# Kernel optimization log

Hardware: AMD Instinct MI355X
Metric: run time of the kernel (lower is better)

## Reference

```python
import jax, jax.numpy as jnp
import numpy as np

N, E, F_IN, H = 100000, 3200000, 256, 32

def gcn_conv(x, src, dst, w, W, b):
    # PyG GCNConv with edge weights and added self-loops (weight 1), symmetric norm
    xw = x @ W                                                # [N, H]
    deg = jax.ops.segment_sum(w, dst, num_segments=N) + 1.0   # includes self-loop
    dis = jax.lax.rsqrt(deg)                                  # deg >= 1, safe
    norm = dis[src] * w * dis[dst]                            # [E]
    agg = jax.ops.segment_sum(norm[:, None] * xw[src], dst, num_segments=N)
    agg = agg + (dis * dis)[:, None] * xw                     # self-loop term
    return agg + b


def setup_inputs() -> dict:
    key = jax.random.key(0)
    ks = jax.random.split(key, 20)
    z = lambda n: jnp.zeros((n,), jnp.float32)
    p = lambda i, shape, s: jax.random.normal(ks[i], shape, jnp.float32) * s
    return {
        "x": jax.random.normal(ks[0], (N, F_IN), jnp.float32),
        "edge_index": jax.random.randint(ks[1], (2, E), 0, N),
        "edge_weight": jax.random.uniform(ks[2], (E,), jnp.float32),
        "prev_hidden_state": jax.random.normal(ks[3], (N, H), jnp.float32),
        # GCNConv weights (stored [in, out]) + post-aggregation biases
        "W_z": p(4, (F_IN, H), 0.05), "b_z": z(H),
        "W_r": p(5, (F_IN, H), 0.05), "b_r": z(H),
        "W_h": p(6, (F_IN, H), 0.05), "b_h": z(H),
        # GRU gate linears Linear(2H, H), stored [2H, H]
        "Lz_W": p(7, (2 * H, H), 0.1), "Lz_b": z(H),
        "Lr_W": p(8, (2 * H, H), 0.1), "Lr_b": z(H),
        "Lh_W": p(9, (2 * H, H), 0.1), "Lh_b": z(H),
        # readout Linear(H, 1)
        "head_W": p(10, (H, 1), 0.1), "head_b": z(1),
    }


def reference(x, edge_index, edge_weight, prev_hidden_state,
              W_z, b_z, W_r, b_r, W_h, b_h,
              Lz_W, Lz_b, Lr_W, Lr_b, Lh_W, Lh_b,
              head_W, head_b):
    src, dst = edge_index[0], edge_index[1]
    Hp = prev_hidden_state
    Z = jax.nn.sigmoid(
        jnp.concatenate([gcn_conv(x, src, dst, edge_weight, W_z, b_z), Hp], 1) @ Lz_W + Lz_b)
    R = jax.nn.sigmoid(
        jnp.concatenate([gcn_conv(x, src, dst, edge_weight, W_r, b_r), Hp], 1) @ Lr_W + Lr_b)
    H_tilde = jnp.tanh(
        jnp.concatenate([gcn_conv(x, src, dst, edge_weight, W_h, b_h), Hp * R], 1) @ Lh_W + Lh_b)
    h = Z * Hp + (1.0 - Z) * H_tilde
    y = jax.nn.relu(h) @ head_W + head_b
    return (y, h)
```

## Files before the change

kernel.cpp:

```cpp
#include <hip/hip_runtime.h>
#include <math.h>

#define N_NODES 100000
#define F_INDIM 256
#define NB 391
#define BCAP 9216

__device__ __forceinline__ unsigned bf16pack(float a, float b) {
  unsigned ua = __float_as_uint(a);
  ua += 0x7FFFu + ((ua >> 16) & 1u);
  unsigned ub = __float_as_uint(b);
  ub += 0x7FFFu + ((ub >> 16) & 1u);
  return (ub & 0xFFFF0000u) | (ua >> 16);
}
__device__ __forceinline__ float lo16(unsigned v) { return __uint_as_float(v << 16); }
__device__ __forceinline__ float hi16(unsigned v) { return __uint_as_float(v & 0xFFFF0000u); }

using bf16x8 = __attribute__((ext_vector_type(8))) short;
using f32x4  = __attribute__((ext_vector_type(4))) float;

__global__ __launch_bounds__(512) void gemm_bin(
    const float* __restrict__ x,
    const float* __restrict__ Wz, const float* __restrict__ Wr, const float* __restrict__ Wh,
    unsigned* __restrict__ XWb,
    const int* __restrict__ ei, const float* __restrict__ w,
    int* __restrict__ bucketCursor, uint2* __restrict__ staged, int E) {
  __shared__ unsigned smem[12672];
  const int t = threadIdx.x;
  const int m = blockIdx.x % 5;
  if (m < 2) {
    int* lc    = (int*)smem;
    int* lbase = (int*)smem + 512;
    if (t < NB) lc[t] = 0;
    __syncthreads();
    const int bid = (blockIdx.x / 5) * 2 + m;
    const int base = bid * 6144;
#pragma unroll
    for (int i = 0; i < 12; i++) {
      int e = base + i * 512 + t;
      if (e < E) atomicAdd(&lc[((unsigned)ei[E + e]) >> 8], 1);
    }
    __syncthreads();
    if (t < NB) {
      int c = lc[t];
      lbase[t] = c ? atomicAdd(&bucketCursor[t], c) : 0;
    }
    __syncthreads();
    if (t < NB) lc[t] = 0;
    __syncthreads();
#pragma unroll
    for (int i = 0; i < 12; i++) {
      int e = base + i * 512 + t;
      if (e < E) {
        unsigned dst = (unsigned)ei[E + e];
        int b = dst >> 8;
        int r = lbase[b] + atomicAdd(&lc[b], 1);
        if (r < BCAP)
          staged[(size_t)b * BCAP + r] =
              make_uint2((unsigned)ei[e] | ((dst & 255u) << 17), __float_as_uint(w[e]));
      }
    }
    return;
  }
  const int gid = (blockIdx.x / 5) * 3 + (m - 2);
  const int row0 = gid * 128;
  if (row0 >= N_NODES) return;
  ushort* sWt = (ushort*)smem;
  {
    const float* Ws[3] = {Wz, Wr, Wh};
#pragma unroll
    for (int mm = 0; mm < 3; mm++) {
      const float* Wp = Ws[mm];
      for (int i = t; i < 8192; i += 512) {
        int k = i >> 5, c = i & 31;
        unsigned uv = __float_as_uint(Wp[i]);
        uv += 0x7FFFu + ((uv >> 16) & 1u);
        sWt[(mm * 32 + c) * 264 + k] = (ushort)(uv >> 16);
      }
    }
  }
  __syncthreads();
  const int wv = t >> 6;
  const int l = t & 63;
  const int nl = l & 15;
  const int kg = l >> 4;
  int arow = row0 + wv * 16 + nl;
  int arowc = arow < N_NODES ? arow : N_NODES - 1;
  f32x4 acc[6];
#pragma unroll
  for (int c = 0; c < 6; c++) acc[c] = (f32x4){0.f, 0.f, 0.f, 0.f};
  const float* xrow = x + (size_t)arowc * F_INDIM + kg * 8;
#pragma unroll
  for (int ks = 0; ks < 8; ks++) {
    float4 xa = *(const float4*)(xrow + ks * 32);
    float4 xb = *(const float4*)(xrow + ks * 32 + 4);
    uint4 au;
    au.x = bf16pack(xa.x, xa.y);
    au.y = bf16pack(xa.z, xa.w);
    au.z = bf16pack(xb.x, xb.y);
    au.w = bf16pack(xb.z, xb.w);
    bf16x8 af = *(bf16x8*)&au;
#pragma unroll
    for (int c = 0; c < 6; c++) {
      const ushort* bp = sWt + (c * 16 + nl) * 264 + ks * 32 + kg * 8;
      bf16x8 bf = *(const bf16x8*)bp;
      acc[c] = __builtin_amdgcn_mfma_f32_16x16x32_bf16(af, bf, acc[c], 0, 0, 0);
    }
  }
#pragma unroll
  for (int c = 0; c < 6; c++) {
#pragma unroll
    for (int r = 0; r < 4; r++) {
      float v = acc[c][r];
      float o = __shfl_xor(v, 1);
      int orow = row0 + wv * 16 + kg * 4 + r;
      if ((nl & 1) == 0 && orow < N_NODES)
        XWb[(size_t)orow * 48 + c * 8 + (nl >> 1)] = bf16pack(v, o);
    }
  }
}

__global__ __launch_bounds__(256) void finalize(
    const uint2* __restrict__ staged, const int* __restrict__ bucketCursor,
    uint2* __restrict__ e2, int* __restrict__ rowstart, int* __restrict__ cntA,
    float* __restrict__ dis) {
  __shared__ int fc[256];
  __shared__ float fd[256];
  __shared__ int fscan[256];
  __shared__ int fcur[256];
  const int t = threadIdx.x;
  const int b = blockIdx.x;
  const size_t lo = (size_t)b * BCAP;
  int M = bucketCursor[b]; if (M > BCAP) M = BCAP;
  fc[t] = 0; fd[t] = 0.f;
  __syncthreads();
  for (int i = t; i < M; i += 256) {
    uint2 ed = staged[lo + i];
    int fl = (ed.x >> 17) & 255;
    atomicAdd(&fc[fl], 1);
    atomicAdd(&fd[fl], __uint_as_float(ed.y));
  }
  __syncthreads();
  int v = fc[t];
  fscan[t] = v;
  __syncthreads();
  for (int off = 1; off < 256; off <<= 1) {
    int xv = (t >= off) ? fscan[t - off] : 0;
    __syncthreads();
    fscan[t] += xv;
    __syncthreads();
  }
  int excl = fscan[t] - v;
  int node = (b << 8) + t;
  if (node < N_NODES) {
    rowstart[node] = (int)lo + excl;
    cntA[node] = v;
    dis[node] = rsqrtf(fd[t] + 1.0f);
  }
  fcur[t] = excl;
  __syncthreads();
  for (int i = t; i < M; i += 256) {
    uint2 ed = staged[lo + i];
    int fl = (ed.x >> 17) & 255;
    int p = atomicAdd(&fcur[fl], 1);
    e2[lo + p] = make_uint2(ed.x & 0x1FFFFu, ed.y);
  }
}

#define FMA8(vv, nn)                                              \
  a0 = fmaf(nn, lo16(vv.x), a0); a1 = fmaf(nn, hi16(vv.x), a1);   \
  a2 = fmaf(nn, lo16(vv.y), a2); a3 = fmaf(nn, hi16(vv.y), a3);   \
  a4 = fmaf(nn, lo16(vv.z), a4); a5 = fmaf(nn, hi16(vv.z), a5);   \
  a6 = fmaf(nn, lo16(vv.w), a6); a7 = fmaf(nn, hi16(vv.w), a7);

__global__ __launch_bounds__(256, 6) void gru_gather(
    const uint2* __restrict__ e2, const int* __restrict__ rowstart,
    const int* __restrict__ cnt, const unsigned* __restrict__ XWb,
    const float* __restrict__ dis, const float* __restrict__ Hp,
    const float* __restrict__ bz, const float* __restrict__ br, const float* __restrict__ bh,
    const float* __restrict__ LzW, const float* __restrict__ Lzb,
    const float* __restrict__ LrW, const float* __restrict__ Lrb,
    const float* __restrict__ LhW, const float* __restrict__ Lhb,
    const float* __restrict__ hW, const float* __restrict__ hb,
    float* __restrict__ outY, float* __restrict__ outH, int N) {
  __shared__ unsigned sLz[1024], sLr[1024], sLh[1024];
  __shared__ float aggTmp[4][5][96];
  __shared__ float sb96[96];
  __shared__ float sLzb[32], sLrb[32], sLhb[32], shW[32];
  __shared__ float2 sg2[4][48];
  __shared__ float shp[4][32], shr[4][32];
  __shared__ float shb;
  const int t = threadIdx.x;
  for (int i = t; i < 1024; i += 256) {
    int jj = i & 31, k2 = i >> 5;
    sLz[i] = bf16pack(LzW[(2 * k2) * 32 + jj], LzW[(2 * k2 + 1) * 32 + jj]);
    sLr[i] = bf16pack(LrW[(2 * k2) * 32 + jj], LrW[(2 * k2 + 1) * 32 + jj]);
    sLh[i] = bf16pack(LhW[(2 * k2) * 32 + jj], LhW[(2 * k2 + 1) * 32 + jj]);
  }
  if (t < 32) {
    sb96[t] = bz[t]; sb96[32 + t] = br[t]; sb96[64 + t] = bh[t];
    sLzb[t] = Lzb[t]; sLrb[t] = Lrb[t]; sLhb[t] = Lhb[t]; shW[t] = hW[t];
  }
  if (t == 0) shb = hb[0];
  __syncthreads();
  const int ws = t >> 6;
  const int l = t & 63;
  const int lp = (l < 48) ? l : 47;
  const int j = l & 31;
  const int half = l >> 5;
  const int sl = (l < 60) ? (l / 12) : 4;
  const int q  = (l < 60) ? (l % 12) : 11;
  const float* sgf = (const float*)&sg2[ws][0];
  int wid = blockIdx.x * 4 + ws;
  int nw = gridDim.x * 4;
  for (int n = wid; n < N; n += nw) {
    const int start = rowstart[n];
    const int c = cnt[n];
    const float d = dis[n];
    float a0 = 0.f, a1 = 0.f, a2 = 0.f, a3 = 0.f;
    float a4 = 0.f, a5 = 0.f, a6 = 0.f, a7 = 0.f;
    for (int e0 = 0; e0 < c; e0 += 60) {
      int srcv = 0; float pw = 0.f;
      if (l < 60 && e0 + l < c) {
        uint2 ed = e2[start + e0 + l];
        srcv = (int)ed.x;
        pw = __uint_as_float(ed.y) * dis[srcv];
      }
      int mm = c - e0; if (mm > 60) mm = 60;
      for (int k0 = 0; k0 < mm; k0 += 10) {
        int iA = k0 + sl, iB = k0 + 5 + sl;
        int sA = __shfl(srcv, iA), sB = __shfl(srcv, iB);
        float nA = __shfl(pw, iA), nB = __shfl(pw, iB);
        uint4 vA = *(const uint4*)(XWb + sA * 48 + (q << 2));
        uint4 vB = *(const uint4*)(XWb + sB * 48 + (q << 2));
        FMA8(vA, nA);
        FMA8(vB, nB);
      }
    }
    if (l < 60) {
      float4* dst4 = (float4*)&aggTmp[ws][sl][q * 8];
      dst4[0] = make_float4(a0, a1, a2, a3);
      dst4[1] = make_float4(a4, a5, a6, a7);
    }
    float g0 = 0.f, g1 = 0.f;
#pragma unroll
    for (int ss = 0; ss < 5; ss++) {
      float2 v2 = *(const float2*)&aggTmp[ws][ss][2 * lp];
      g0 += v2.x; g1 += v2.y;
    }
    g0 *= d; g1 *= d;
    {
      unsigned v = XWb[n * 48 + lp];
      float d2 = d * d;
      g0 = fmaf(d2, lo16(v), g0) + sb96[2 * lp];
      g1 = fmaf(d2, hi16(v), g1) + sb96[2 * lp + 1];
    }
    if (l < 48) sg2[ws][l] = make_float2(g0, g1);
    float hpj = 0.f;
    if (l < 32) { hpj = Hp[(size_t)n * 32 + l]; shp[ws][l] = hpj; }
    const unsigned* Wm = half ? sLr : sLz;
    const float* gsel = half ? (sgf + 32) : sgf;
    float val = half ? sLrb[j] : sLzb[j];
#pragma unroll
    for (int k2 = 0; k2 < 16; k2++) {
      unsigned wv = Wm[k2 * 32 + j];
      val = fmaf(gsel[2 * k2],     lo16(wv), val);
      val = fmaf(gsel[2 * k2 + 1], hi16(wv), val);
    }
#pragma unroll
    for (int k2 = 16; k2 < 32; k2++) {
      unsigned wv = Wm[k2 * 32 + j];
      val = fmaf(shp[ws][2 * k2 - 32], lo16(wv), val);
      val = fmaf(shp[ws][2 * k2 - 31], hi16(wv), val);
    }
    float gate = 1.f / (1.f + __expf(-val));
    if (half) shr[ws][j] = shp[ws][j] * gate;
    float s = half ? 0.f : sLhb[j];
#pragma unroll
    for (int k2 = 0; k2 < 16; k2++) {
      int kk2 = half ? (k2 + 16) : k2;
      unsigned wv = sLh[kk2 * 32 + j];
      float x0 = half ? shr[ws][2 * k2]     : sgf[64 + 2 * k2];
      float x1 = half ? shr[ws][2 * k2 + 1] : sgf[64 + 2 * k2 + 1];
      s = fmaf(x0, lo16(wv), s);
      s = fmaf(x1, hi16(wv), s);
    }
    s += __shfl_xor(s, 32);
    if (!half) {
      float ht = tanhf(s);
      float h = gate * hpj + (1.f - gate) * ht;
      outH[(size_t)n * 32 + j] = h;
      float cacc = fmaxf(h, 0.f) * shW[j];
#pragma unroll
      for (int off = 16; off > 0; off >>= 1) cacc += __shfl_xor(cacc, off, 32);
      if (j == 0) outY[n] = cacc + shb;
    }
  }
}

extern "C" void kernel_launch(void* const* d_in, const int* in_sizes, int n_in,
                              void* d_out, int out_size, void* d_ws, size_t ws_size,
                              hipStream_t stream) {
  const float* x    = (const float*)d_in[0];
  const int*   ei   = (const int*)d_in[1];
  const float* w    = (const float*)d_in[2];
  const float* Hp   = (const float*)d_in[3];
  const float* Wz   = (const float*)d_in[4];
  const float* bz   = (const float*)d_in[5];
  const float* Wr   = (const float*)d_in[6];
  const float* br   = (const float*)d_in[7];
  const float* Wh   = (const float*)d_in[8];
  const float* bh   = (const float*)d_in[9];
  const float* LzW  = (const float*)d_in[10];
  const float* Lzb  = (const float*)d_in[11];
  const float* LrW  = (const float*)d_in[12];
  const float* Lrb  = (const float*)d_in[13];
  const float* LhW  = (const float*)d_in[14];
  const float* Lhb  = (const float*)d_in[15];
  const float* hW   = (const float*)d_in[16];
  const float* hb   = (const float*)d_in[17];

  const int N = N_NODES;
  const int E = in_sizes[2];

  char* p = (char*)d_ws;
  unsigned* XWb   = (unsigned*)p;  p += (size_t)(N * 48 + 64) * 4;
  uint2*    staged= (uint2*)p;     p += (size_t)NB * BCAP * 8;
  uint2*    e2    = (uint2*)p;     p += (size_t)NB * BCAP * 8;
  int* rowstart   = (int*)p;       p += (size_t)N * 4;
  int* cnt        = (int*)p;       p += (size_t)N * 4;
  float* dis      = (float*)p;     p += (size_t)N * 4;
  int* bucketCursor = (int*)p;     p += (NB + 1) * 4;

  float* outY = (float*)d_out;
  float* outH = outY + N;

  hipMemsetAsync(bucketCursor, 0, (NB + 1) * sizeof(int), stream);

  gemm_bin<<<1305, 512, 0, stream>>>(x, Wz, Wr, Wh, XWb, ei, w,
                                     bucketCursor, staged, E);
  finalize<<<NB, 256, 0, stream>>>(staged, bucketCursor, e2, rowstart, cnt, dis);
  gru_gather<<<1536, 256, 0, stream>>>(e2, rowstart, cnt, XWb, dis, Hp,
                                       bz, br, bh,
                                       LzW, Lzb, LrW, Lrb, LhW, Lhb,
                                       hW, hb, outY, outH, N);
}
```

Before: 232.0 us.

## Gather neighbor features from an FP8 copy of XW instead of BF16

The finalize kernel now also converts the BF16 XW matrix into a packed FP8 (e4m3) copy. The edge gather reads 24 bytes per source row instead of 48 and decodes them with hardware fp8-to-f32 conversion. Lanes are remapped so 6 lanes cover a row and 10 edges are processed per step, with a cross-lane shuffle reduction before the shared-memory sum. The aim is to halve the dominant random-gather traffic, at the cost of an extra conversion pass and a notable loss of precision in the aggregated features.

```diff
diff --git a/kernel.cpp b/kernel.cpp
--- a/kernel.cpp
+++ b/kernel.cpp
@@ -18,6 +18,7 @@
 
 using bf16x8 = __attribute__((ext_vector_type(8))) short;
 using f32x4  = __attribute__((ext_vector_type(4))) float;
+using f32x2  = __attribute__((ext_vector_type(2))) float;
 
 __global__ __launch_bounds__(512) void gemm_bin(
     const float* __restrict__ x,
@@ -123,7 +124,8 @@
 __global__ __launch_bounds__(256) void finalize(
     const uint2* __restrict__ staged, const int* __restrict__ bucketCursor,
     uint2* __restrict__ e2, int* __restrict__ rowstart, int* __restrict__ cntA,
-    float* __restrict__ dis) {
+    float* __restrict__ dis,
+    const unsigned* __restrict__ XWb, unsigned* __restrict__ XW8) {
   __shared__ int fc[256];
   __shared__ float fd[256];
   __shared__ int fscan[256];
@@ -165,17 +167,22 @@
     int p = atomicAdd(&fcur[fl], 1);
     e2[lo + p] = make_uint2(ed.x & 0x1FFFFu, ed.y);
   }
-}
-
-#define FMA8(vv, nn)                                              \
-  a0 = fmaf(nn, lo16(vv.x), a0); a1 = fmaf(nn, hi16(vv.x), a1);   \
-  a2 = fmaf(nn, lo16(vv.y), a2); a3 = fmaf(nn, hi16(vv.y), a3);   \
-  a4 = fmaf(nn, lo16(vv.z), a4); a5 = fmaf(nn, hi16(vv.z), a5);   \
-  a6 = fmaf(nn, lo16(vv.w), a6); a7 = fmaf(nn, hi16(vv.w), a7);
+  for (int i = t; i < 256 * 24; i += 256) {
+    int row = (b << 8) + (i / 24);
+    if (row >= N_NODES) break;
+    int od = i % 24;
+    unsigned u0 = XWb[(size_t)row * 48 + od * 2];
+    unsigned u1 = XWb[(size_t)row * 48 + od * 2 + 1];
+    int r = __builtin_amdgcn_cvt_pk_fp8_f32(lo16(u0), hi16(u0), 0, false);
+    r = __builtin_amdgcn_cvt_pk_fp8_f32(lo16(u1), hi16(u1), r, true);
+    XW8[(size_t)row * 24 + od] = (unsigned)r;
+  }
+}
 
 __global__ __launch_bounds__(256, 6) void gru_gather(
     const uint2* __restrict__ e2, const int* __restrict__ rowstart,
     const int* __restrict__ cnt, const unsigned* __restrict__ XWb,
+    const unsigned* __restrict__ XW8,
     const float* __restrict__ dis, const float* __restrict__ Hp,
     const float* __restrict__ bz, const float* __restrict__ br, const float* __restrict__ bh,
     const float* __restrict__ LzW, const float* __restrict__ Lzb,
@@ -208,8 +215,8 @@
   const int lp = (l < 48) ? l : 47;
   const int j = l & 31;
   const int half = l >> 5;
-  const int sl = (l < 60) ? (l / 12) : 4;
-  const int q  = (l < 60) ? (l % 12) : 11;
+  const int s10 = (l < 60) ? (l / 6) : 9;
+  const int q6  = (l < 60) ? (l % 6) : 5;
   const float* sgf = (const float*)&sg2[ws][0];
   int wid = blockIdx.x * 4 + ws;
   int nw = gridDim.x * 4;
@@ -217,30 +224,53 @@
     const int start = rowstart[n];
     const int c = cnt[n];
     const float d = dis[n];
-    float a0 = 0.f, a1 = 0.f, a2 = 0.f, a3 = 0.f;
-    float a4 = 0.f, a5 = 0.f, a6 = 0.f, a7 = 0.f;
+    float a[16];
+#pragma unroll
+    for (int i = 0; i < 16; i++) a[i] = 0.f;
     for (int e0 = 0; e0 < c; e0 += 60) {
-      int srcv = 0; float pw = 0.f;
+      unsigned srcv = 0; float pw = 0.f;
       if (l < 60 && e0 + l < c) {
         uint2 ed = e2[start + e0 + l];
-        srcv = (int)ed.x;
+        srcv = ed.x;
         pw = __uint_as_float(ed.y) * dis[srcv];
       }
       int mm = c - e0; if (mm > 60) mm = 60;
-      for (int k0 = 0; k0 < mm; k0 += 10) {
-        int iA = k0 + sl, iB = k0 + 5 + sl;
-        int sA = __shfl(srcv, iA), sB = __shfl(srcv, iB);
+      for (int k0 = 0; k0 < mm; k0 += 20) {
+        int iA = k0 + s10, iB = k0 + 10 + s10;
+        unsigned sA = __shfl(srcv, iA), sB = __shfl(srcv, iB);
         float nA = __shfl(pw, iA), nB = __shfl(pw, iB);
-        uint4 vA = *(const uint4*)(XWb + sA * 48 + (q << 2));
-        uint4 vB = *(const uint4*)(XWb + sB * 48 + (q << 2));
-        FMA8(vA, nA);
-        FMA8(vB, nB);
+        uint4 vA = *(const uint4*)(XW8 + (size_t)sA * 24 + (q6 << 2));
+        uint4 vB = *(const uint4*)(XW8 + (size_t)sB * 24 + (q6 << 2));
+#pragma unroll
+        for (int dd = 0; dd < 4; dd++) {
+          unsigned wd = (dd == 0) ? vA.x : (dd == 1) ? vA.y : (dd == 2) ? vA.z : vA.w;
+          f32x2 f01 = __builtin_amdgcn_cvt_pk_f32_fp8((int)wd, false);
+          f32x2 f23 = __builtin_amdgcn_cvt_pk_f32_fp8((int)wd, true);
+          a[dd * 4 + 0] = fmaf(nA, f01[0], a[dd * 4 + 0]);
+          a[dd * 4 + 1] = fmaf(nA, f01[1], a[dd * 4 + 1]);
+          a[dd * 4 + 2] = fmaf(nA, f23[0], a[dd * 4 + 2]);
+          a[dd * 4 + 3] = fmaf(nA, f23[1], a[dd * 4 + 3]);
+        }
+#pragma unroll
+        for (int dd = 0; dd < 4; dd++) {
+          unsigned wd = (dd == 0) ? vB.x : (dd == 1) ? vB.y : (dd == 2) ? vB.z : vB.w;
+          f32x2 f01 = __builtin_amdgcn_cvt_pk_f32_fp8((int)wd, false);
+          f32x2 f23 = __builtin_amdgcn_cvt_pk_f32_fp8((int)wd, true);
+          a[dd * 4 + 0] = fmaf(nB, f01[0], a[dd * 4 + 0]);
+          a[dd * 4 + 1] = fmaf(nB, f01[1], a[dd * 4 + 1]);
+          a[dd * 4 + 2] = fmaf(nB, f23[0], a[dd * 4 + 2]);
+          a[dd * 4 + 3] = fmaf(nB, f23[1], a[dd * 4 + 3]);
+        }
       }
     }
-    if (l < 60) {
-      float4* dst4 = (float4*)&aggTmp[ws][sl][q * 8];
-      dst4[0] = make_float4(a0, a1, a2, a3);
-      dst4[1] = make_float4(a4, a5, a6, a7);
+#pragma unroll
+    for (int i = 0; i < 16; i++) a[i] += __shfl(a[i], l + 30);
+    if (l < 30) {
+      float4* dst4 = (float4*)&aggTmp[ws][s10][q6 * 16];
+      dst4[0] = make_float4(a[0], a[1], a[2], a[3]);
+      dst4[1] = make_float4(a[4], a[5], a[6], a[7]);
+      dst4[2] = make_float4(a[8], a[9], a[10], a[11]);
+      dst4[3] = make_float4(a[12], a[13], a[14], a[15]);
     }
     float g0 = 0.f, g1 = 0.f;
 #pragma unroll
@@ -250,7 +280,7 @@
     }
     g0 *= d; g1 *= d;
     {
-      unsigned v = XWb[n * 48 + lp];
+      unsigned v = XWb[(size_t)n * 48 + lp];
       float d2 = d * d;
       g0 = fmaf(d2, lo16(v), g0) + sb96[2 * lp];
       g1 = fmaf(d2, hi16(v), g1) + sb96[2 * lp + 1];
@@ -325,6 +355,7 @@
 
   char* p = (char*)d_ws;
   unsigned* XWb   = (unsigned*)p;  p += (size_t)(N * 48 + 64) * 4;
+  unsigned* XW8   = (unsigned*)p;  p += (size_t)(N * 24 + 64) * 4;
   uint2*    staged= (uint2*)p;     p += (size_t)NB * BCAP * 8;
   uint2*    e2    = (uint2*)p;     p += (size_t)NB * BCAP * 8;
   int* rowstart   = (int*)p;       p += (size_t)N * 4;
@@ -339,8 +370,9 @@
 
   gemm_bin<<<1305, 512, 0, stream>>>(x, Wz, Wr, Wh, XWb, ei, w,
                                      bucketCursor, staged, E);
-  finalize<<<NB, 256, 0, stream>>>(staged, bucketCursor, e2, rowstart, cnt, dis);
-  gru_gather<<<1536, 256, 0, stream>>>(e2, rowstart, cnt, XWb, dis, Hp,
+  finalize<<<NB, 256, 0, stream>>>(staged, bucketCursor, e2, rowstart, cnt, dis,
+                                   XWb, XW8);
+  gru_gather<<<1536, 256, 0, stream>>>(e2, rowstart, cnt, XWb, XW8, dis, Hp,
                                        bz, br, bh,
                                        LzW, Lzb, LrW, Lrb, LhW, Lhb,
                                        hW, hb, outY, outH, N);
```

Measured after the change: 306.8 us. +32.3%, slower.

## Move edge binning to its own kernel and co-schedule finalize with the GEMM

Applied to the files above, without the earlier changes.

Edge binning now runs as a standalone kernel that keeps dst indices in registers instead of reloading them. The bucket finalize pass (count, scan, scatter) is merged into the GEMM kernel, interleaved by block index, so finalize work overlaps the x@W GEMM rather than running as a separate launch afterwards. Finalize blocks now use 512 threads with half idle during the scan. The kernel count stays the same, but binning no longer overlaps the GEMM. The gather also switches to size_t index arithmetic.

```diff
diff --git a/kernel.cpp b/kernel.cpp
--- a/kernel.cpp
+++ b/kernel.cpp
@@ -19,50 +19,101 @@
 using bf16x8 = __attribute__((ext_vector_type(8))) short;
 using f32x4  = __attribute__((ext_vector_type(4))) float;
 
-__global__ __launch_bounds__(512) void gemm_bin(
+__global__ __launch_bounds__(512) void bin_kernel(
+    const int* __restrict__ ei, const float* __restrict__ w,
+    int* __restrict__ bucketCursor, uint2* __restrict__ staged, int E) {
+  __shared__ int lc[512];
+  __shared__ int lbase[512];
+  const int t = threadIdx.x;
+  if (t < NB) lc[t] = 0;
+  __syncthreads();
+  const int base = blockIdx.x * 6144;
+  int dstv[12];
+#pragma unroll
+  for (int i = 0; i < 12; i++) {
+    int e = base + i * 512 + t;
+    dstv[i] = (e < E) ? ei[E + e] : -1;
+    if (dstv[i] >= 0) atomicAdd(&lc[((unsigned)dstv[i]) >> 8], 1);
+  }
+  __syncthreads();
+  if (t < NB) {
+    int c = lc[t];
+    lbase[t] = c ? atomicAdd(&bucketCursor[t], c) : 0;
+  }
+  __syncthreads();
+  if (t < NB) lc[t] = 0;
+  __syncthreads();
+#pragma unroll
+  for (int i = 0; i < 12; i++) {
+    int e = base + i * 512 + t;
+    if (dstv[i] >= 0) {
+      unsigned dst = (unsigned)dstv[i];
+      int b = dst >> 8;
+      int r = lbase[b] + atomicAdd(&lc[b], 1);
+      if (r < BCAP)
+        staged[(size_t)b * BCAP + r] =
+            make_uint2((unsigned)ei[e] | ((dst & 255u) << 17), __float_as_uint(w[e]));
+    }
+  }
+}
+
+__global__ __launch_bounds__(512) void gemm_fin(
     const float* __restrict__ x,
     const float* __restrict__ Wz, const float* __restrict__ Wr, const float* __restrict__ Wh,
     unsigned* __restrict__ XWb,
-    const int* __restrict__ ei, const float* __restrict__ w,
-    int* __restrict__ bucketCursor, uint2* __restrict__ staged, int E) {
+    const uint2* __restrict__ staged, const int* __restrict__ bucketCursor,
+    uint2* __restrict__ e2, int* __restrict__ rowstart, int* __restrict__ cntA,
+    float* __restrict__ dis) {
   __shared__ unsigned smem[12672];
   const int t = threadIdx.x;
-  const int m = blockIdx.x % 5;
-  if (m < 2) {
-    int* lc    = (int*)smem;
-    int* lbase = (int*)smem + 512;
-    if (t < NB) lc[t] = 0;
+  const int m = blockIdx.x % 3;
+  if (m == 0) {
+    int*   fc    = (int*)smem;
+    float* fd    = (float*)smem + 256;
+    int*   fscan = (int*)smem + 512;
+    int*   fcur  = (int*)smem + 768;
+    const int b = blockIdx.x / 3;
+    if (b >= NB) return;
+    const size_t lo = (size_t)b * BCAP;
+    int M = bucketCursor[b]; if (M > BCAP) M = BCAP;
+    if (t < 256) { fc[t] = 0; fd[t] = 0.f; }
     __syncthreads();
-    const int bid = (blockIdx.x / 5) * 2 + m;
-    const int base = bid * 6144;
-#pragma unroll
-    for (int i = 0; i < 12; i++) {
-      int e = base + i * 512 + t;
-      if (e < E) atomicAdd(&lc[((unsigned)ei[E + e]) >> 8], 1);
+    for (int i = t; i < M; i += 512) {
+      uint2 ed = staged[lo + i];
+      int fl = (ed.x >> 17) & 255;
+      atomicAdd(&fc[fl], 1);
+      atomicAdd(&fd[fl], __uint_as_float(ed.y));
     }
     __syncthreads();
-    if (t < NB) {
-      int c = lc[t];
-      lbase[t] = c ? atomicAdd(&bucketCursor[t], c) : 0;
-    }
+    int v = (t < 256) ? fc[t] : 0;
+    if (t < 256) fscan[t] = v;
     __syncthreads();
-    if (t < NB) lc[t] = 0;
+    for (int off = 1; off < 256; off <<= 1) {
+      int xv = (t >= off && t < 256) ? fscan[t - off] : 0;
+      __syncthreads();
+      if (t < 256) fscan[t] += xv;
+      __syncthreads();
+    }
+    if (t < 256) {
+      int excl = fscan[t] - v;
+      int node = (b << 8) + t;
+      if (node < N_NODES) {
+        rowstart[node] = (int)lo + excl;
+        cntA[node] = v;
+        dis[node] = rsqrtf(fd[t] + 1.0f);
+      }
+      fcur[t] = excl;
+    }
     __syncthreads();
-#pragma unroll
-    for (int i = 0; i < 12; i++) {
-      int e = base + i * 512 + t;
-      if (e < E) {
-        unsigned dst = (unsigned)ei[E + e];
-        int b = dst >> 8;
-        int r = lbase[b] + atomicAdd(&lc[b], 1);
-        if (r < BCAP)
-          staged[(size_t)b * BCAP + r] =
-              make_uint2((unsigned)ei[e] | ((dst & 255u) << 17), __float_as_uint(w[e]));
-      }
+    for (int i = t; i < M; i += 512) {
+      uint2 ed = staged[lo + i];
+      int fl = (ed.x >> 17) & 255;
+      int p = atomicAdd(&fcur[fl], 1);
+      e2[lo + p] = make_uint2(ed.x & 0x1FFFFu, ed.y);
     }
     return;
   }
-  const int gid = (blockIdx.x / 5) * 3 + (m - 2);
+  const int gid = (blockIdx.x / 3) * 2 + (m - 1);
   const int row0 = gid * 128;
   if (row0 >= N_NODES) return;
   ushort* sWt = (ushort*)smem;
@@ -117,53 +168,6 @@
       if ((nl & 1) == 0 && orow < N_NODES)
         XWb[(size_t)orow * 48 + c * 8 + (nl >> 1)] = bf16pack(v, o);
     }
-  }
-}
-
-__global__ __launch_bounds__(256) void finalize(
-    const uint2* __restrict__ staged, const int* __restrict__ bucketCursor,
-    uint2* __restrict__ e2, int* __restrict__ rowstart, int* __restrict__ cntA,
-    float* __restrict__ dis) {
-  __shared__ int fc[256];
-  __shared__ float fd[256];
-  __shared__ int fscan[256];
-  __shared__ int fcur[256];
-  const int t = threadIdx.x;
-  const int b = blockIdx.x;
-  const size_t lo = (size_t)b * BCAP;
-  int M = bucketCursor[b]; if (M > BCAP) M = BCAP;
-  fc[t] = 0; fd[t] = 0.f;
-  __syncthreads();
-  for (int i = t; i < M; i += 256) {
-    uint2 ed = staged[lo + i];
-    int fl = (ed.x >> 17) & 255;
-    atomicAdd(&fc[fl], 1);
-    atomicAdd(&fd[fl], __uint_as_float(ed.y));
-  }
-  __syncthreads();
-  int v = fc[t];
-  fscan[t] = v;
-  __syncthreads();
-  for (int off = 1; off < 256; off <<= 1) {
-    int xv = (t >= off) ? fscan[t - off] : 0;
-    __syncthreads();
-    fscan[t] += xv;
-    __syncthreads();
-  }
-  int excl = fscan[t] - v;
-  int node = (b << 8) + t;
-  if (node < N_NODES) {
-    rowstart[node] = (int)lo + excl;
-    cntA[node] = v;
-    dis[node] = rsqrtf(fd[t] + 1.0f);
-  }
-  fcur[t] = excl;
-  __syncthreads();
-  for (int i = t; i < M; i += 256) {
-    uint2 ed = staged[lo + i];
-    int fl = (ed.x >> 17) & 255;
-    int p = atomicAdd(&fcur[fl], 1);
-    e2[lo + p] = make_uint2(ed.x & 0x1FFFFu, ed.y);
   }
 }
 
@@ -231,8 +235,8 @@
         int iA = k0 + sl, iB = k0 + 5 + sl;
         int sA = __shfl(srcv, iA), sB = __shfl(srcv, iB);
         float nA = __shfl(pw, iA), nB = __shfl(pw, iB);
-        uint4 vA = *(const uint4*)(XWb + sA * 48 + (q << 2));
-        uint4 vB = *(const uint4*)(XWb + sB * 48 + (q << 2));
+        uint4 vA = *(const uint4*)(XWb + (size_t)sA * 48 + (q << 2));
+        uint4 vB = *(const uint4*)(XWb + (size_t)sB * 48 + (q << 2));
         FMA8(vA, nA);
         FMA8(vB, nB);
       }
@@ -250,7 +254,7 @@
     }
     g0 *= d; g1 *= d;
     {
-      unsigned v = XWb[n * 48 + lp];
+      unsigned v = XWb[(size_t)n * 48 + lp];
       float d2 = d * d;
       g0 = fmaf(d2, lo16(v), g0) + sb96[2 * lp];
       g1 = fmaf(d2, hi16(v), g1) + sb96[2 * lp + 1];
@@ -337,9 +341,10 @@
 
   hipMemsetAsync(bucketCursor, 0, (NB + 1) * sizeof(int), stream);
 
-  gemm_bin<<<1305, 512, 0, stream>>>(x, Wz, Wr, Wh, XWb, ei, w,
-                                     bucketCursor, staged, E);
-  finalize<<<NB, 256, 0, stream>>>(staged, bucketCursor, e2, rowstart, cnt, dis);
+  const int nBinBlocks = (E + 6143) / 6144;
+  bin_kernel<<<nBinBlocks, 512, 0, stream>>>(ei, w, bucketCursor, staged, E);
+  gemm_fin<<<1173, 512, 0, stream>>>(x, Wz, Wr, Wh, XWb,
+                                     staged, bucketCursor, e2, rowstart, cnt, dis);
   gru_gather<<<1536, 256, 0, stream>>>(e2, rowstart, cnt, XWb, dis, Hp,
                                        bz, br, bh,
                                        LzW, Lzb, LrW, Lrb, LhW, Lhb,
```

Result: slower. 250.6 us (+8.0%).
